# Performance work log

Measured on AMD Instinct MI355X. Metric: run time of the kernel, lower is better.

The kernel has to match this reference:

```python
import jax, jax.numpy as jnp
import numpy as np


def setup_inputs() -> dict:
    key = jax.random.key(0)
    k_x, k_q, k_k, k_v = jax.random.split(key, 4)
    seq_len, d_in, d_out = 4096, 1024, 1024
    x = jax.random.normal(k_x, (seq_len, d_in), dtype=jnp.float32)
    # torch nn.Linear weights are [d_out, d_in]; applied as x @ W.T
    scale = 1.0 / np.sqrt(d_in)
    Wq = jax.random.uniform(k_q, (d_out, d_in), jnp.float32, -scale, scale)
    Wk = jax.random.uniform(k_k, (d_out, d_in), jnp.float32, -scale, scale)
    Wv = jax.random.uniform(k_v, (d_out, d_in), jnp.float32, -scale, scale)
    return {"x": x, "Wq": Wq, "Wk": Wk, "Wv": Wv}


def reference(x, Wq, Wk, Wv):
    # x: [S, d_in]; Wq/Wk/Wv: [d_out, d_in]
    queries = x @ Wq.T          # [S, d_out]
    keys = x @ Wk.T             # [S, d_out]
    values = x @ Wv.T           # [S, d_out]
    d_k = keys.shape[-1]
    attn_scores = queries @ keys.T                      # [S, S]
    attn_weights = jax.nn.softmax(attn_scores / jnp.sqrt(jnp.float32(d_k)), axis=-1)
    S = attn_scores.shape[0]
    tril = jnp.tril(jnp.ones((S, S), dtype=attn_weights.dtype))
    masked = tril * attn_weights
    masked_norm = masked / jnp.sum(masked, axis=-1, keepdims=True)
    context_vec = masked_norm @ values                  # [S, d_out]
    return context_vec
```

## Files before the change

kernel.cpp:

```cpp
#include <hip/hip_runtime.h>
#include <hip/hip_bf16.h>


typedef __bf16 bf16_t;
typedef __bf16 bf16x4v __attribute__((ext_vector_type(4)));
typedef __bf16 bf16x8 __attribute__((ext_vector_type(8)));
typedef float f32x4 __attribute__((ext_vector_type(4)));
typedef unsigned char u8;
typedef long long i64_t;

#define AS1 __attribute__((address_space(1)))
#define AS3 __attribute__((address_space(3)))
#define WAIT_VMCNT(N) asm volatile("s_waitcnt vmcnt(" #N ")" ::: "memory")
#define BARRIER_RAW() asm volatile("s_barrier" ::: "memory")

__device__ __forceinline__ void async_copy16(const void* g, void* l) {
    __builtin_amdgcn_global_load_lds((AS1 void*)(g), (AS3 void*)(l), 16, 0, 0);
}

__device__ __forceinline__ u8 f32_to_fp8(float v) {
    return (u8)(__builtin_amdgcn_cvt_pk_fp8_f32(v, v, 0, false) & 0xff);
}

__device__ __forceinline__ void store_conv(float* p, float v) { *p = v; }
__device__ __forceinline__ void store_conv(bf16_t* p, float v) { *p = (bf16_t)v; }
__device__ __forceinline__ void store_conv(u8* p, float v) { *p = f32_to_fp8(v); }

__device__ __forceinline__ float sum32(const float* p) {
    const f32x4* v = (const f32x4*)p;
    float s = 0.f;
#pragma unroll
    for (int u = 0; u < 8; ++u) {
        f32x4 a = v[u];
        s += a[0] + a[1] + a[2] + a[3];
    }
    return s;
}

template <int EPI, typename OutT>
__device__ __forceinline__ void gemm_tile_bf16(const bf16_t* __restrict__ A, int lda,
                                               const bf16_t* __restrict__ B, int ldb,
                                               OutT* __restrict__ C, int ldc,
                                               int kb0, int kb1, float alpha,
                                               char* __restrict__ smem,
                                               const float* __restrict__ inv) {
    constexpr int BK = 64;
    bf16_t* As = (bf16_t*)smem;
    bf16_t* Bs = (bf16_t*)(smem + 32768);
    const int tid = threadIdx.x;
    const int lane = tid & 63, wave = tid >> 6;
    const int wm = wave >> 1, wn = wave & 1;
    const int q = lane >> 4, l16 = lane & 15;

    f32x4 acc[4][4] = {};

    const bf16_t* aSrc[4];
    const bf16_t* bSrc[4];
    int ldsOff[4];
#pragma unroll
    for (int it = 0; it < 4; ++it) {
        int c = it * 256 + tid;
        int r = c >> 3, b = c & 7;
        int sb = b ^ (r & 7);
        aSrc[it] = A + (size_t)r * lda + sb * 8;
        bSrc[it] = B + (size_t)r * ldb + sb * 8;
        ldsOff[it] = c * 8;
    }

    {
        const int k0 = kb0 * BK;
#pragma unroll
        for (int it = 0; it < 4; ++it) async_copy16(aSrc[it] + k0, &As[ldsOff[it]]);
#pragma unroll
        for (int it = 0; it < 4; ++it) async_copy16(bSrc[it] + k0, &Bs[ldsOff[it]]);
    }

    int cur = 0;
    for (int kb = kb0; kb < kb1; ++kb) {
        if (kb + 1 < kb1) {
            const int k0 = (kb + 1) * BK;
            const int boff = (cur ^ 1) * 8192;
#pragma unroll
            for (int it = 0; it < 4; ++it) async_copy16(aSrc[it] + k0, &As[boff + ldsOff[it]]);
#pragma unroll
            for (int it = 0; it < 4; ++it) async_copy16(bSrc[it] + k0, &Bs[boff + ldsOff[it]]);
            WAIT_VMCNT(8);
        } else {
            WAIT_VMCNT(0);
        }
        __builtin_amdgcn_sched_barrier(0);
        BARRIER_RAW();
        const bf16_t* Ab = As + cur * 8192;
        const bf16_t* Bb = Bs + cur * 8192;
        __builtin_amdgcn_s_setprio(1);
#pragma unroll
        for (int k2 = 0; k2 < 2; ++k2) {
            bf16x8 af[4], bfr[4];
#pragma unroll
            for (int mt = 0; mt < 4; ++mt) {
                int m = wm * 64 + mt * 16 + l16;
                int blk = (k2 * 4 + q) ^ (m & 7);
                af[mt] = *(const bf16x8*)&Ab[m * BK + blk * 8];
            }
#pragma unroll
            for (int nt = 0; nt < 4; ++nt) {
                int nn = wn * 64 + nt * 16 + l16;
                int blk = (k2 * 4 + q) ^ (nn & 7);
                bfr[nt] = *(const bf16x8*)&Bb[nn * BK + blk * 8];
            }
#pragma unroll
            for (int mt = 0; mt < 4; ++mt)
#pragma unroll
                for (int nt = 0; nt < 4; ++nt)
                    acc[mt][nt] = __builtin_amdgcn_mfma_f32_16x16x32_bf16(
                        af[mt], bfr[nt], acc[mt][nt], 0, 0, 0);
        }
        __builtin_amdgcn_s_setprio(0);
        BARRIER_RAW();
        cur ^= 1;
    }

    constexpr int S = (int)sizeof(OutT);
    constexpr int RB = 128 * S;
    const int row0 = wm * 64, col0 = wn * 64;
#pragma unroll
    for (int mt = 0; mt < 4; ++mt)
#pragma unroll
        for (int nt = 0; nt < 4; ++nt)
#pragma unroll
            for (int r = 0; r < 4; ++r) {
                int lr = row0 + mt * 16 + q * 4 + r;
                int lc = col0 + nt * 16 + l16;
                float v = acc[mt][nt][r];
                v = (EPI == 2) ? v * inv[lr] : v * alpha;
                int cb = (lc * S) >> 4;
                int sw = cb ^ ((lr >> 2) & 7);
                store_conv((OutT*)(smem + lr * RB + (sw << 4) + ((lc * S) & 15)), v);
            }
    __syncthreads();
#pragma unroll
    for (int p = 0; p < 4 * S; ++p) {
        int g = p * 4096 + tid * 16;
        int r = g / RB;
        int wb = g & (RB - 1);
        int sc = (wb >> 4) ^ ((r >> 2) & 7);
        f32x4 val = *(const f32x4*)(smem + r * RB + (sc << 4));
        *(f32x4*)((char*)C + (size_t)r * ((size_t)ldc * S) + wb) = val;
    }
}

__device__ __forceinline__ void gemm_tile_bf16_sb(const bf16_t* __restrict__ A, int lda,
                                                  const bf16_t* __restrict__ B, int ldb,
                                                  bf16_t* __restrict__ C, int ldc,
                                                  int kb1, char* __restrict__ smem) {
    constexpr int BK = 64;
    bf16_t* As = (bf16_t*)smem;
    bf16_t* Bs = (bf16_t*)(smem + 16384);
    const int tid = threadIdx.x;
    const int lane = tid & 63, wave = tid >> 6;
    const int wm = wave >> 1, wn = wave & 1;
    const int q = lane >> 4, l16 = lane & 15;

    f32x4 acc[4][4] = {};

    const bf16_t* aSrc[4];
    const bf16_t* bSrc[4];
    int ldsOff[4];
#pragma unroll
    for (int it = 0; it < 4; ++it) {
        int c = it * 256 + tid;
        int r = c >> 3, b = c & 7;
        int sb = b ^ (r & 7);
        aSrc[it] = A + (size_t)r * lda + sb * 8;
        bSrc[it] = B + (size_t)r * ldb + sb * 8;
        ldsOff[it] = c * 8;
    }

    for (int kb = 0; kb < kb1; ++kb) {
        const int k0 = kb * BK;
#pragma unroll
        for (int it = 0; it < 4; ++it) async_copy16(aSrc[it] + k0, &As[ldsOff[it]]);
#pragma unroll
        for (int it = 0; it < 4; ++it) async_copy16(bSrc[it] + k0, &Bs[ldsOff[it]]);
        __syncthreads();
        __builtin_amdgcn_s_setprio(1);
#pragma unroll
        for (int k2 = 0; k2 < 2; ++k2) {
            bf16x8 af[4], bfr[4];
#pragma unroll
            for (int mt = 0; mt < 4; ++mt) {
                int m = wm * 64 + mt * 16 + l16;
                int blk = (k2 * 4 + q) ^ (m & 7);
                af[mt] = *(const bf16x8*)&As[m * BK + blk * 8];
            }
#pragma unroll
            for (int nt = 0; nt < 4; ++nt) {
                int nn = wn * 64 + nt * 16 + l16;
                int blk = (k2 * 4 + q) ^ (nn & 7);
                bfr[nt] = *(const bf16x8*)&Bs[nn * BK + blk * 8];
            }
#pragma unroll
            for (int mt = 0; mt < 4; ++mt)
#pragma unroll
                for (int nt = 0; nt < 4; ++nt)
                    acc[mt][nt] = __builtin_amdgcn_mfma_f32_16x16x32_bf16(
                        af[mt], bfr[nt], acc[mt][nt], 0, 0, 0);
        }
        __builtin_amdgcn_s_setprio(0);
        __syncthreads();
    }

    constexpr int RB = 256;
    const int row0 = wm * 64, col0 = wn * 64;
#pragma unroll
    for (int mt = 0; mt < 4; ++mt)
#pragma unroll
        for (int nt = 0; nt < 4; ++nt)
#pragma unroll
            for (int r = 0; r < 4; ++r) {
                int lr = row0 + mt * 16 + q * 4 + r;
                int lc = col0 + nt * 16 + l16;
                int cb = (lc * 2) >> 4;
                int sw = cb ^ ((lr >> 2) & 7);
                *(bf16_t*)(smem + lr * RB + (sw << 4) + ((lc * 2) & 15)) =
                    (bf16_t)acc[mt][nt][r];
            }
    __syncthreads();
#pragma unroll
    for (int p = 0; p < 8; ++p) {
        int g = p * 4096 + tid * 16;
        int r = g >> 8, wb = g & 255;
        int sc = (wb >> 4) ^ ((r >> 2) & 7);
        f32x4 val = *(const f32x4*)(smem + r * RB + (sc << 4));
        *(f32x4*)((char*)C + (size_t)r * ((size_t)ldc * 2) + wb) = val;
    }
}

__device__ __forceinline__ void scores_tile_fp8_sb(const u8* __restrict__ A, int lda,
                                                   const u8* __restrict__ B, int ldb,
                                                   bf16_t* __restrict__ C, int ldc,
                                                   float alpha, char* __restrict__ smem,
                                                   float* __restrict__ partial,
                                                   int gr0, int gc0) {
    u8* As = (u8*)smem;
    u8* Bs = (u8*)(smem + 16384);
    const int tid = threadIdx.x;
    const int lane = tid & 63, wave = tid >> 6;
    const int wm = wave >> 1, wn = wave & 1;
    const int q = lane >> 4, l16 = lane & 15;

    f32x4 acc[4][4] = {};

    const u8* aSrc[4];
    const u8* bSrc[4];
    int ldsOff[4];
#pragma unroll
    for (int it = 0; it < 4; ++it) {
        int c = it * 256 + tid;
        int r = c >> 3, b = c & 7;
        int sb = b ^ (r & 7);
        aSrc[it] = A + (size_t)r * lda + sb * 16;
        bSrc[it] = B + (size_t)r * ldb + sb * 16;
        ldsOff[it] = c * 16;
    }

    for (int kb = 0; kb < 8; ++kb) {
        const int k0 = kb * 128;
#pragma unroll
        for (int it = 0; it < 4; ++it) async_copy16(aSrc[it] + k0, &As[ldsOff[it]]);
#pragma unroll
        for (int it = 0; it < 4; ++it) async_copy16(bSrc[it] + k0, &Bs[ldsOff[it]]);
        __syncthreads();
        __builtin_amdgcn_s_setprio(1);
#pragma unroll
        for (int k2 = 0; k2 < 4; ++k2) {
            i64_t af[4], bfr[4];
            const int cb = 2 * k2 + (q >> 1), co = (q & 1) * 8;
#pragma unroll
            for (int mt = 0; mt < 4; ++mt) {
                int m = wm * 64 + mt * 16 + l16;
                af[mt] = *(const i64_t*)&As[m * 128 + ((cb ^ (m & 7)) << 4) + co];
            }
#pragma unroll
            for (int nt = 0; nt < 4; ++nt) {
                int nn = wn * 64 + nt * 16 + l16;
                bfr[nt] = *(const i64_t*)&Bs[nn * 128 + ((cb ^ (nn & 7)) << 4) + co];
            }
#pragma unroll
            for (int mt = 0; mt < 4; ++mt)
#pragma unroll
                for (int nt = 0; nt < 4; ++nt)
                    acc[mt][nt] = __builtin_amdgcn_mfma_f32_16x16x32_fp8_fp8(
                        af[mt], bfr[nt], acc[mt][nt], 0, 0, 0);
        }
        __builtin_amdgcn_s_setprio(0);
        __syncthreads();
    }

    float* sred = (float*)(smem + 32768);
    const int row0 = wm * 64, col0 = wn * 64;
    float esum[4][4];
#pragma unroll
    for (int mt = 0; mt < 4; ++mt)
#pragma unroll
        for (int r = 0; r < 4; ++r) esum[mt][r] = 0.f;
#pragma unroll
    for (int mt = 0; mt < 4; ++mt)
#pragma unroll
        for (int nt = 0; nt < 4; ++nt)
#pragma unroll
            for (int r = 0; r < 4; ++r) {
                int lr = row0 + mt * 16 + q * 4 + r;
                int lc = col0 + nt * 16 + l16;
                float pe = (gc0 + lc > gr0 + lr) ? 0.f : __expf(acc[mt][nt][r] * alpha);
                esum[mt][r] += pe;
                int sw = (lc >> 3) ^ ((lr >> 2) & 7);
                *(bf16_t*)(smem + lr * 256 + (sw << 4) + ((lc * 2) & 15)) = (bf16_t)pe;
            }
#pragma unroll
    for (int mt = 0; mt < 4; ++mt)
#pragma unroll
        for (int r = 0; r < 4; ++r) {
#pragma unroll
            for (int off = 1; off < 16; off <<= 1)
                esum[mt][r] += __shfl_xor(esum[mt][r], off, 64);
            if (l16 == 0) sred[(row0 + mt * 16 + q * 4 + r) * 2 + wn] = esum[mt][r];
        }
    __syncthreads();
#pragma unroll
    for (int p = 0; p < 8; ++p) {
        int g = p * 4096 + tid * 16;
        int r = g >> 8;
        int wb = g & 255;
        int sc = (wb >> 4) ^ ((r >> 2) & 7);
        f32x4 val = *(const f32x4*)(smem + r * 256 + (sc << 4));
        *(f32x4*)((char*)C + (size_t)r * ((size_t)ldc * 2) + wb) = val;
    }
    if (tid < 128) partial[(size_t)tid * 32] = sred[tid * 2] + sred[tid * 2 + 1];
}

__device__ __forceinline__ void scores_tile_fp8_sb_half(
        const u8* __restrict__ A, int lda, const u8* __restrict__ B, int ldb,
        bf16_t* __restrict__ C, int ldc, float alpha, char* __restrict__ smem,
        float* __restrict__ partial, int gr0, int gc0, int half) {
    u8* As = (u8*)smem;
    u8* Bs = (u8*)(smem + 16384);
    const int tid = threadIdx.x;
    const int lane = tid & 63, wave = tid >> 6;
    const int wm = wave >> 1, wn = wave & 1;
    const int q = lane >> 4, l16 = lane & 15;

    f32x4 acc[2][4] = {};

    const u8* aSrc[2];
    const u8* bSrc[4];
    int aOff[2], bOff[4];
#pragma unroll
    for (int it = 0; it < 2; ++it) {
        int c = it * 256 + tid;
        int r = c >> 3, b = c & 7;
        int sb = b ^ (r & 7);
        int srcRow = r + 32 * half + 32 * it;
        aSrc[it] = A + (size_t)srcRow * lda + sb * 16;
        aOff[it] = c * 16;
    }
#pragma unroll
    for (int it = 0; it < 4; ++it) {
        int c = it * 256 + tid;
        int r = c >> 3, b = c & 7;
        int sb = b ^ (r & 7);
        bSrc[it] = B + (size_t)r * ldb + sb * 16;
        bOff[it] = c * 16;
    }

    for (int kb = 0; kb < 8; ++kb) {
        const int k0 = kb * 128;
#pragma unroll
        for (int it = 0; it < 2; ++it) async_copy16(aSrc[it] + k0, &As[aOff[it]]);
#pragma unroll
        for (int it = 0; it < 4; ++it) async_copy16(bSrc[it] + k0, &Bs[bOff[it]]);
        __syncthreads();
        __builtin_amdgcn_s_setprio(1);
#pragma unroll
        for (int k2 = 0; k2 < 4; ++k2) {
            i64_t af[2], bfr[4];
            const int cb = 2 * k2 + (q >> 1), co = (q & 1) * 8;
#pragma unroll
            for (int mt = 0; mt < 2; ++mt) {
                int m = wm * 32 + mt * 16 + l16;
                af[mt] = *(const i64_t*)&As[m * 128 + ((cb ^ (m & 7)) << 4) + co];
            }
#pragma unroll
            for (int nt = 0; nt < 4; ++nt) {
                int nn = wn * 64 + nt * 16 + l16;
                bfr[nt] = *(const i64_t*)&Bs[nn * 128 + ((cb ^ (nn & 7)) << 4) + co];
            }
#pragma unroll
            for (int mt = 0; mt < 2; ++mt)
#pragma unroll
                for (int nt = 0; nt < 4; ++nt)
                    acc[mt][nt] = __builtin_amdgcn_mfma_f32_16x16x32_fp8_fp8(
                        af[mt], bfr[nt], acc[mt][nt], 0, 0, 0);
        }
        __builtin_amdgcn_s_setprio(0);
        __syncthreads();
    }

    float* sred = (float*)(smem + 32768);
    const int col0 = wn * 64;
    float esum[2][4];
#pragma unroll
    for (int mt = 0; mt < 2; ++mt)
#pragma unroll
        for (int r = 0; r < 4; ++r) esum[mt][r] = 0.f;
#pragma unroll
    for (int mt = 0; mt < 2; ++mt)
#pragma unroll
        for (int nt = 0; nt < 4; ++nt)
#pragma unroll
            for (int r = 0; r < 4; ++r) {
                int cr = wm * 32 + mt * 16 + q * 4 + r;
                int trow = ((cr >> 5) << 6) + 32 * half + (cr & 31);
                int lc = col0 + nt * 16 + l16;
                float pe = (gc0 + lc > gr0 + trow) ? 0.f : __expf(acc[mt][nt][r] * alpha);
                esum[mt][r] += pe;
                int sw = (lc >> 3) ^ ((cr >> 2) & 7);
                *(bf16_t*)(smem + cr * 256 + (sw << 4) + ((lc * 2) & 15)) = (bf16_t)pe;
            }
#pragma unroll
    for (int mt = 0; mt < 2; ++mt)
#pragma unroll
        for (int r = 0; r < 4; ++r) {
#pragma unroll
            for (int off = 1; off < 16; off <<= 1)
                esum[mt][r] += __shfl_xor(esum[mt][r], off, 64);
            if (l16 == 0)
                sred[(wm * 32 + mt * 16 + q * 4 + r) * 2 + wn] = esum[mt][r];
        }
    __syncthreads();
#pragma unroll
    for (int p = 0; p < 4; ++p) {
        int g = p * 4096 + tid * 16;
        int cr = g >> 8, wb = g & 255;
        int sc = (wb >> 4) ^ ((cr >> 2) & 7);
        f32x4 val = *(const f32x4*)(smem + cr * 256 + (sc << 4));
        int trow = ((cr >> 5) << 6) + 32 * half + (cr & 31);
        *(f32x4*)((char*)C + (size_t)trow * ((size_t)ldc * 2) + wb) = val;
    }
    if (tid < 64) {
        int trow = ((tid >> 5) << 6) + 32 * half + (tid & 31);
        partial[(size_t)trow * 32] = sred[tid * 2] + sred[tid * 2 + 1];
    }
}

__global__ __launch_bounds__(256) void k_qkv(const bf16_t* __restrict__ xb,
                                             const bf16_t* __restrict__ wqk,
                                             u8* __restrict__ qk) {
    __shared__ __attribute__((aligned(16))) char smem[65536];
    int b = blockIdx.x;
    int bm = b & 31, bn = b >> 5;
    gemm_tile_bf16<0, u8>(xb + (size_t)bm * 128 * 1024, 1024,
                          wqk + (size_t)bn * 128 * 1024, 1024,
                          qk + (size_t)bm * 128 * 2048 + bn * 128, 2048,
                          0, 16, 1.f, smem, nullptr);
}

__global__ __launch_bounds__(256, 4) void k_sv(const bf16_t* __restrict__ xb,
                                               const bf16_t* __restrict__ wvb,
                                               const u8* __restrict__ qk,
                                               bf16_t* __restrict__ vt,
                                               bf16_t* __restrict__ P,
                                               float* __restrict__ rowsum_part) {
    __shared__ __attribute__((aligned(16))) char smem[33792];
    int b = blockIdx.x;
    if (b < 256) {
        int bm = b & 7, bn = b >> 3;
        gemm_tile_bf16_sb(wvb + (size_t)bm * 128 * 1024, 1024,
                          xb + (size_t)bn * 128 * 1024, 1024,
                          vt + (size_t)bm * 128 * 4096 + bn * 128, 4096,
                          16, smem);
        return;
    }
    if (b < 768) {
        int t = b - 256;
        int bm = (int)((sqrtf(8.f * (float)t + 1.f) - 1.f) * 0.5f);
        while (bm * (bm + 1) / 2 > t) --bm;
        while ((bm + 1) * (bm + 2) / 2 <= t) ++bm;
        int bn = t - bm * (bm + 1) / 2;
        scores_tile_fp8_sb(qk + (size_t)bm * 128 * 2048, 2048,
                           qk + 1024 + (size_t)bn * 128 * 2048, 2048,
                           P + (size_t)bm * 128 * 4096 + bn * 128, 4096,
                           0.03125f, smem,
                           rowsum_part + (size_t)bm * 128 * 32 + bn,
                           bm * 128, bn * 128);
        if (bn == bm) {
            float* rp = rowsum_part + (size_t)bm * 128 * 32;
            int tid = threadIdx.x;
            for (int r = tid >> 4; r < 128; r += 16)
                for (int u = bm + 1 + (tid & 15); u < 32; u += 16)
                    rp[r * 32 + u] = 0.f;
        }
        return;
    }
    int j = b - 768;
    int bn = 16 + (j >> 1);
    int half = j & 1;
    scores_tile_fp8_sb_half(qk + (size_t)31 * 128 * 2048, 2048,
                            qk + 1024 + (size_t)bn * 128 * 2048, 2048,
                            P + (size_t)31 * 128 * 4096 + bn * 128, 4096,
                            0.03125f, smem,
                            rowsum_part + (size_t)31 * 128 * 32 + bn,
                            31 * 128, bn * 128, half);
}

__global__ __launch_bounds__(256) void k_pv(const bf16_t* __restrict__ P,
                                            const bf16_t* __restrict__ vt,
                                            const float* __restrict__ rowsum_part,
                                            float* __restrict__ out,
                                            float* __restrict__ partials) {
    __shared__ __attribute__((aligned(16))) char smem[65536];
    __shared__ float sInv[128];
    int b = blockIdx.x;
    int bn = b & 7, g = b >> 3;
    int bm, s, ns;
    if (g < 11)      { bm = g;                  s = 0;             ns = 1; }
    else if (g < 33) { bm = 11 + (g - 11) / 2;  s = (g - 11) % 2;  ns = 2; }
    else             { bm = 22 + (g - 33) / 3;  s = (g - 33) % 3;  ns = 3; }
    int nk = 2 * (bm + 1);
    int kb0 = s * nk / ns;
    int kb1 = (s + 1) * nk / ns;

    const bf16_t* A = P + (size_t)bm * 128 * 4096;
    const bf16_t* B = vt + (size_t)bn * 128 * 4096;
    if (ns == 1) {
        int tid = threadIdx.x;
        if (tid < 128)
            sInv[tid] = 1.f / sum32(rowsum_part + (size_t)(bm * 128 + tid) * 32);
        gemm_tile_bf16<2, float>(A, 4096, B, 4096,
                                 out + (size_t)bm * 128 * 1024 + bn * 128, 1024,
                                 kb0, kb1, 1.f, smem, sInv);
    } else {
        int cum = (bm < 22) ? (bm - 11) * 2 : 22 + (bm - 22) * 3;
        gemm_tile_bf16<0, float>(A, 4096, B, 4096,
                                 partials + ((size_t)(cum + s) * 8 + bn) * 16384, 128,
                                 kb0, kb1, 1.f, smem, nullptr);
    }
}

__global__ __launch_bounds__(256) void k_reduce(const float* __restrict__ partials,
                                                const float* __restrict__ rowsum_part,
                                                float* __restrict__ out) {
    int b = blockIdx.x;
    int t = b % 168, p = b / 168;
    int bm = 11 + t % 21, bn = t / 21;
    int ns = (bm < 22) ? 2 : 3;
    int cum = (bm < 22) ? (bm - 11) * 2 : 22 + (bm - 22) * 3;
    __shared__ float sInv[8];
    int tid = threadIdx.x;
    if (tid < 8) {
        int row = bm * 128 + p * 8 + tid;
        sInv[tid] = 1.f / sum32(rowsum_part + (size_t)row * 32);
    }
    __syncthreads();

    int idx = p * 1024 + tid * 4;
    int lr = idx >> 7, lc = idx & 127;
    float sx = 0.f, sy = 0.f, sz = 0.f, sw = 0.f;
    for (int u = 0; u < ns; ++u) {
        const float4 v = *(const float4*)(partials + ((size_t)(cum + u) * 8 + bn) * 16384 + idx);
        sx += v.x; sy += v.y; sz += v.z; sw += v.w;
    }
    float inv = sInv[lr - p * 8];
    float4 o = {sx * inv, sy * inv, sz * inv, sw * inv};
    *(float4*)(out + (size_t)(bm * 128 + lr) * 1024 + bn * 128 + lc) = o;
}

__global__ __launch_bounds__(256) void cast_to_bf16(const float* __restrict__ x,
                                                    const float* __restrict__ Wq,
                                                    const float* __restrict__ Wk,
                                                    const float* __restrict__ Wv,
                                                    bf16_t* __restrict__ xb,
                                                    bf16_t* __restrict__ wqk,
                                                    bf16_t* __restrict__ wv) {
    const int NX = (4096 * 1024) / 4;
    const int NW = (1024 * 1024) / 4;
    int idx = blockIdx.x * 256 + threadIdx.x;
    const float* src;
    bf16_t* dst;
    int off;
    if (idx < NX) {
        src = x; dst = xb; off = idx;
    } else if (idx < NX + NW) {
        src = Wq; dst = wqk; off = idx - NX;
    } else if (idx < NX + 2 * NW) {
        src = Wk; dst = wqk + (size_t)NW * 4; off = idx - NX - NW;
    } else {
        src = Wv; dst = wv; off = idx - NX - 2 * NW;
    }
    float4 f = ((const float4*)src)[off];
    bf16x4v o;
    o.x = (bf16_t)f.x; o.y = (bf16_t)f.y; o.z = (bf16_t)f.z; o.w = (bf16_t)f.w;
    *(bf16x4v*)(dst + (size_t)off * 4) = o;
}

extern "C" void kernel_launch(void* const* d_in, const int* in_sizes, int n_in,
                              void* d_out, int out_size, void* d_ws, size_t ws_size,
                              hipStream_t stream) {
    (void)in_sizes; (void)n_in; (void)out_size; (void)ws_size;
    const float* x  = (const float*)d_in[0];
    const float* Wq = (const float*)d_in[1];
    const float* Wk = (const float*)d_in[2];
    const float* Wv = (const float*)d_in[3];
    float* out = (float*)d_out;

    char* ws = (char*)d_ws;
    bf16_t* xb   = (bf16_t*)(ws + (size_t)0);
    bf16_t* wqk  = (bf16_t*)(ws + ((size_t)8 << 20));
    bf16_t* wvb  = (bf16_t*)(ws + ((size_t)12 << 20));
    u8*     qk   = (u8*)(ws + ((size_t)14 << 20));
    bf16_t* vt   = (bf16_t*)(ws + ((size_t)22 << 20));
    bf16_t* P    = (bf16_t*)(ws + ((size_t)30 << 20));
    float* rowsp = (float*)(ws + ((size_t)62 << 20));
    float* parts = (float*)(ws + ((size_t)64 << 20));

    cast_to_bf16<<<7168, 256, 0, stream>>>(x, Wq, Wk, Wv, xb, wqk, wvb);

    k_qkv<<<512, 256, 0, stream>>>(xb, wqk, qk);

    k_sv<<<800, 256, 0, stream>>>(xb, wvb, qk, vt, P, rowsp);

    k_pv<<<504, 256, 0, stream>>>(P, vt, rowsp, out, parts);
    k_reduce<<<2688, 256, 0, stream>>>(parts, rowsp, out);
}
```

Measured before the change: 165.4 us.

## Rewrite QK projection GEMM with 256x128 tiles and triple-buffered A pipeline

Replaces the generic 128x128 tile GEMM for the Q/K projection with a dedicated 512-thread kernel computing 256x128 tiles. A is triple-buffered and B double-buffered in LDS via async global-to-LDS copies, and the prefetches are interleaved between two halves of the MFMA work, with setprio raising priority around the MFMAs. Larger tiles cut redundant loads of B and launch 256 blocks instead of 512, at the cost of 128KB of LDS per block and fewer blocks to fill the CUs.

```diff
diff --git a/kernel.cpp b/kernel.cpp
--- a/kernel.cpp
+++ b/kernel.cpp
@@ -12,6 +12,7 @@
 #define AS1 __attribute__((address_space(1)))
 #define AS3 __attribute__((address_space(3)))
 #define WAIT_VMCNT(N) asm volatile("s_waitcnt vmcnt(" #N ")" ::: "memory")
+#define WAIT_LGKM0() asm volatile("s_waitcnt lgkmcnt(0)" ::: "memory")
 #define BARRIER_RAW() asm volatile("s_barrier" ::: "memory")
 
 __device__ __forceinline__ void async_copy16(const void* g, void* l) {
@@ -453,16 +454,153 @@
     }
 }
 
-__global__ __launch_bounds__(256) void k_qkv(const bf16_t* __restrict__ xb,
-                                             const bf16_t* __restrict__ wqk,
-                                             u8* __restrict__ qk) {
-    __shared__ __attribute__((aligned(16))) char smem[65536];
-    int b = blockIdx.x;
-    int bm = b & 31, bn = b >> 5;
-    gemm_tile_bf16<0, u8>(xb + (size_t)bm * 128 * 1024, 1024,
-                          wqk + (size_t)bn * 128 * 1024, 1024,
-                          qk + (size_t)bm * 128 * 2048 + bn * 128, 2048,
-                          0, 16, 1.f, smem, nullptr);
+__global__ __launch_bounds__(512, 2) void k_qkv(const bf16_t* __restrict__ xb,
+                                                const bf16_t* __restrict__ wqk,
+                                                u8* __restrict__ qk) {
+    __shared__ __attribute__((aligned(16))) char smem[131072];
+    const int b = blockIdx.x;
+    const int bm = b & 15, bn = b >> 4;
+    const bf16_t* A = xb + (size_t)bm * 256 * 1024;
+    const bf16_t* Bw = wqk + (size_t)bn * 128 * 1024;
+    u8* C = qk + (size_t)bm * 256 * 2048 + bn * 128;
+
+    const int tid = threadIdx.x;
+    const int lane = tid & 63, wave = tid >> 6;
+    const int wm = wave >> 2, wn = wave & 3;
+    const int q = lane >> 4, l16 = lane & 15;
+
+    f32x4 acc[8][2] = {};
+
+    const bf16_t* aS[4]; int aO[4];
+    const bf16_t* bS[2]; int bO[2];
+#pragma unroll
+    for (int pp = 0; pp < 4; ++pp) {
+        int g = pp * 512 + tid, r = g >> 3, c8 = g & 7, sb = c8 ^ (r & 7);
+        aS[pp] = A + (size_t)r * 1024 + sb * 8;
+        aO[pp] = g * 16;
+    }
+#pragma unroll
+    for (int pp = 0; pp < 2; ++pp) {
+        int g = pp * 512 + tid, r = g >> 3, c8 = g & 7, sb = c8 ^ (r & 7);
+        bS[pp] = Bw + (size_t)r * 1024 + sb * 8;
+        bO[pp] = g * 16;
+    }
+
+#pragma unroll
+    for (int kb = 0; kb < 2; ++kb) {
+        char* as = smem + kb * 32768;
+        char* bs = smem + 98304 + kb * 16384;
+        const int k0 = kb * 64;
+        async_copy16(aS[0] + k0, as + aO[0]);
+        async_copy16(aS[1] + k0, as + aO[1]);
+        async_copy16(aS[2] + k0, as + aO[2]);
+        async_copy16(aS[3] + k0, as + aO[3]);
+        async_copy16(bS[0] + k0, bs + bO[0]);
+        async_copy16(bS[1] + k0, bs + bO[1]);
+    }
+    WAIT_VMCNT(6);
+    __builtin_amdgcn_sched_barrier(0);
+    BARRIER_RAW();
+
+    for (int kb = 0; kb < 16; ++kb) {
+        const int asl = kb - (kb / 3) * 3;
+        const int nsl = (kb + 2) - ((kb + 2) / 3) * 3;
+        const bf16_t* Ab = (const bf16_t*)(smem + asl * 32768);
+        const bf16_t* Bb = (const bf16_t*)(smem + 98304 + (kb & 1) * 16384);
+        char* nA = smem + nsl * 32768;
+        char* nB = smem + 98304 + (kb & 1) * 16384;
+        const int kn = (kb + 2) * 64;
+        const bool pre = (kb + 2) < 16;
+
+        bf16x8 bf[2][2], af[4][2];
+#pragma unroll
+        for (int nt = 0; nt < 2; ++nt)
+#pragma unroll
+            for (int k2 = 0; k2 < 2; ++k2) {
+                int nn = wn * 32 + nt * 16 + l16;
+                int blk = (k2 * 4 + q) ^ (nn & 7);
+                bf[nt][k2] = *(const bf16x8*)&Bb[nn * 64 + blk * 8];
+            }
+#pragma unroll
+        for (int mt = 0; mt < 4; ++mt)
+#pragma unroll
+            for (int k2 = 0; k2 < 2; ++k2) {
+                int m = wm * 128 + mt * 16 + l16;
+                int blk = (k2 * 4 + q) ^ (m & 7);
+                af[mt][k2] = *(const bf16x8*)&Ab[m * 64 + blk * 8];
+            }
+        if (pre) {
+            async_copy16(aS[0] + kn, nA + aO[0]);
+            async_copy16(aS[1] + kn, nA + aO[1]);
+        }
+        WAIT_LGKM0();
+        __builtin_amdgcn_sched_barrier(0);
+        BARRIER_RAW();
+        __builtin_amdgcn_s_setprio(1);
+#pragma unroll
+        for (int mt = 0; mt < 4; ++mt)
+#pragma unroll
+            for (int nt = 0; nt < 2; ++nt)
+#pragma unroll
+                for (int k2 = 0; k2 < 2; ++k2)
+                    acc[mt][nt] = __builtin_amdgcn_mfma_f32_16x16x32_bf16(
+                        af[mt][k2], bf[nt][k2], acc[mt][nt], 0, 0, 0);
+        __builtin_amdgcn_s_setprio(0);
+
+#pragma unroll
+        for (int mt = 0; mt < 4; ++mt)
+#pragma unroll
+            for (int k2 = 0; k2 < 2; ++k2) {
+                int m = wm * 128 + (4 + mt) * 16 + l16;
+                int blk = (k2 * 4 + q) ^ (m & 7);
+                af[mt][k2] = *(const bf16x8*)&Ab[m * 64 + blk * 8];
+            }
+        if (pre) {
+            async_copy16(aS[2] + kn, nA + aO[2]);
+            async_copy16(aS[3] + kn, nA + aO[3]);
+            async_copy16(bS[0] + kn, nB + bO[0]);
+            async_copy16(bS[1] + kn, nB + bO[1]);
+        }
+        WAIT_LGKM0();
+        __builtin_amdgcn_sched_barrier(0);
+        __builtin_amdgcn_s_setprio(1);
+#pragma unroll
+        for (int mt = 0; mt < 4; ++mt)
+#pragma unroll
+            for (int nt = 0; nt < 2; ++nt)
+#pragma unroll
+                for (int k2 = 0; k2 < 2; ++k2)
+                    acc[4 + mt][nt] = __builtin_amdgcn_mfma_f32_16x16x32_bf16(
+                        af[mt][k2], bf[nt][k2], acc[4 + mt][nt], 0, 0, 0);
+        __builtin_amdgcn_s_setprio(0);
+
+        if (pre) { WAIT_VMCNT(6); } else { WAIT_VMCNT(0); }
+        __builtin_amdgcn_sched_barrier(0);
+        BARRIER_RAW();
+    }
+
+#pragma unroll
+    for (int mt = 0; mt < 8; ++mt)
+#pragma unroll
+        for (int nt = 0; nt < 2; ++nt)
+#pragma unroll
+            for (int r = 0; r < 4; ++r) {
+                int lr = wm * 128 + mt * 16 + q * 4 + r;
+                int lc = wn * 32 + nt * 16 + l16;
+                int cb = lc >> 4;
+                int sw = cb ^ ((lr >> 2) & 7);
+                *(u8*)(smem + lr * 128 + (sw << 4) + (lc & 15)) =
+                    f32_to_fp8(acc[mt][nt][r]);
+            }
+    __syncthreads();
+#pragma unroll
+    for (int p = 0; p < 4; ++p) {
+        int g = p * 8192 + tid * 16;
+        int r = g >> 7, wb = g & 127;
+        int sc = (wb >> 4) ^ ((r >> 2) & 7);
+        f32x4 val = *(const f32x4*)(smem + r * 128 + (sc << 4));
+        *(f32x4*)((char*)C + (size_t)r * 2048 + wb) = val;
+    }
 }
 
 __global__ __launch_bounds__(256, 4) void k_sv(const bf16_t* __restrict__ xb,
@@ -625,7 +763,7 @@
 
     cast_to_bf16<<<7168, 256, 0, stream>>>(x, Wq, Wk, Wv, xb, wqk, wvb);
 
-    k_qkv<<<512, 256, 0, stream>>>(xb, wqk, qk);
+    k_qkv<<<256, 512, 0, stream>>>(xb, wqk, qk);
 
     k_sv<<<800, 256, 0, stream>>>(xb, wvb, qk, vt, P, rowsp);
 
```

After: 164.7 us. About the same (-0.4%).
